# Kernel optimization log

Hardware: AMD Instinct MI355X
Metric: run time of the kernel (lower is better)

## Reference

```python
import jax, jax.numpy as jnp
import numpy as np

B, T, P = 256, 1024, 32
HOME = 0  # home_idx from init_kwargs


def setup_inputs() -> dict:
    key = jax.random.key(0)
    k1, k2 = jax.random.split(key, 2)
    U = jax.random.normal(k1, (B, T, P), dtype=jnp.float32)
    A = jax.random.uniform(k2, (P, P), dtype=jnp.float32, minval=-0.01, maxval=0.01)
    bias = jnp.zeros((P,), dtype=jnp.float32)
    return {"unary_logits_btp": U, "A": A, "bias": bias}


def reference(unary_logits_btp, A, bias):
    """Constrained Viterbi decode (enforce at least one non-home state).
    State is (purpose p, visited-nonhome flag v in {0,1}). Returns paths (B,T) int32."""
    U = unary_logits_btp + bias  # (B,T,P), bias broadcast as in decode()
    Bn, Tn, Pn = U.shape
    NEG = jnp.finfo(U.dtype).min / 4
    is_home = jnp.arange(Pn) == HOME  # (P,)

    # t=0: v=0 only at home, v=1 only at non-home
    d0 = jnp.where(is_home, U[:, 0], NEG)
    d1 = jnp.where(is_home, NEG, U[:, 0])
    delta0 = jnp.stack([d0, d1], axis=-1)  # (B,P,2)

    def step(delta, U_t):
        # prev{v}[b, q, p] = delta[b, q, v] + A[q, p]
        prev0 = delta[:, :, 0][:, :, None] + A  # (B,P,P)
        prev1 = delta[:, :, 1][:, :, None] + A
        a0 = jnp.argmax(prev0, axis=1).astype(jnp.int32)
        v0 = jnp.max(prev0, axis=1)  # (B,P)
        a1 = jnp.argmax(prev1, axis=1).astype(jnp.int32)
        v1 = jnp.max(prev1, axis=1)
        use1 = v1 > v0  # strict >, matching torch.where(val_from1 > val_from0, ...)
        bval = jnp.where(use1, v1, v0)
        bq = jnp.where(use1, a1, a0)
        bv = use1.astype(jnp.int32)
        # next v=0 reachable only at home (from prev v=0)
        dn0 = jnp.where(is_home, v0 + U_t, NEG)
        # next v=1: home from prev v=1; non-home from best of prev v=0/v=1
        dn1 = jnp.where(is_home, v1, bval) + U_t
        p1 = jnp.where(is_home, a1, bq)
        vv1 = jnp.where(is_home, 1, bv).astype(jnp.int32)
        delta_new = jnp.stack([dn0, dn1], axis=-1)          # (B,P,2)
        psi_p = jnp.stack([a0, p1], axis=-1)                # (B,P,2) best prev purpose
        psi_v = jnp.stack([jnp.zeros_like(vv1), vv1], -1)   # (B,P,2) best prev flag
        return delta_new, (psi_p, psi_v)

    Us = jnp.swapaxes(U, 0, 1)  # (T,B,P)
    delta_T, (psi_p, psi_v) = jax.lax.scan(step, delta0, Us[1:])  # psi_*: (T-1,B,P,2)

    last_p = jnp.argmax(delta_T[:, :, 1], axis=1).astype(jnp.int32)  # (B,)
    b_idx = jnp.arange(Bn)

    def back(carry, psi):
        y, v = carry  # (B,), (B,)
        pp, pv = psi  # (B,P,2)
        py = pp[b_idx, y, v]
        nv = pv[b_idx, y, v]
        return (py, nv), py

    _, ys = jax.lax.scan(back, (last_p, jnp.ones((Bn,), jnp.int32)), (psi_p, psi_v),
                         reverse=True)  # ys: (T-1,B) with ys[t] = y[t]
    paths = jnp.concatenate([jnp.swapaxes(ys, 0, 1), last_p[:, None]], axis=1)  # (B,T)
    return paths
```

## Files before the change

### kernel.cpp

```cpp
#include <hip/hip_runtime.h>

#define T_LEN 1024
#define P_DIM 32
#define HOME_IDX 0
#define NCHUNK 32
#define CHUNK 32


__launch_bounds__(1024, 1)
__global__ void crf_viterbi_kernel(const float* __restrict__ U,
                                   const float* __restrict__ A,
                                   const float* __restrict__ bias,
                                   int* __restrict__ out)
{
    __shared__ unsigned char spsi[(T_LEN - 1) * P_DIM];
    __shared__ unsigned char Mmap[NCHUNK * P_DIM];
    __shared__ unsigned char ent[NCHUNK];
    __shared__ int last_p_sh;

    const int tid = threadIdx.x;
    const int b   = blockIdx.x;
    int* __restrict__ outb = out + (size_t)b * T_LEN;

    if (tid < 64) {
        const int lane = tid;
        const int p    = lane & 31;
        const int h    = lane >> 5;
        const float NEG = -(3.4028234663852886e38f / 4.0f);

        float Areg[16];
#pragma unroll
        for (int j = 0; j < 16; ++j)
            Areg[j] = A[(16 * h + j) * P_DIM + p];
        const float A0p    = A[p];
        const float A00    = A[0];
        const float bias_p = bias[p];
        const float bias0  = bias[0];
        const int   qb     = h << 6;
        const bool  is_home = (p == HOME_IDX);

        const float* __restrict__ Ub = U + (size_t)b * T_LEN * P_DIM;

        const float u00 = Ub[p] + bias_p;
        float delta1  = is_home ? NEG : u00;
        float delta0h = Ub[HOME_IDX] + bias0;

        float L0 = Ub[1 * P_DIM + p];
        float L1 = Ub[2 * P_DIM + p];
        float L2 = Ub[3 * P_DIM + p];
        float L3 = Ub[4 * P_DIM + p];

        float Ut_n = L0 + bias_p;
        float u0_n = __shfl(Ut_n, 0);

#define STEP(t, Lc, Lr) do {                                                   \
    const float Ut  = Ut_n;                                                    \
    const float u0c = u0_n;                                                    \
    Ut_n = (Lc) + bias_p;                                                      \
    u0_n = __shfl(Ut_n, 0);                                                    \
    { int tn = (t) + 4; if (tn > T_LEN - 1) tn = T_LEN - 1;                    \
      (Lr) = Ub[(size_t)tn * P_DIM + p]; }                                     \
    const int dsrc = __float_as_int(delta1);                                   \
    float c[16];                                                               \
    _Pragma("unroll")                                                          \
    for (int j = 0; j < 16; ++j)                                               \
        c[j] = __int_as_float(__builtin_amdgcn_ds_bpermute(qb + 4 * j, dsrc))  \
               + Areg[j];                                                      \
                           \
    const float g0 = fmaxf(fmaxf(c[0],  c[1]),  c[2]);                         \
    const float g1 = fmaxf(fmaxf(c[3],  c[4]),  c[5]);                         \
    const float g2 = fmaxf(fmaxf(c[6],  c[7]),  c[8]);                         \
    const float g3 = fmaxf(fmaxf(c[9],  c[10]), c[11]);                        \
    const float g4 = fmaxf(fmaxf(c[12], c[13]), c[14]);                        \
    const float h0 = fmaxf(fmaxf(g0, g1), g2);                                 \
    const float h1 = fmaxf(fmaxf(g3, g4), c[15]);                              \
    const float bv = fmaxf(h0, h1);                                            \
    const float ovv = __shfl_xor(bv, 32);                                      \
    const float v1  = fmaxf(bv, ovv);                                          \
    const float v0  = delta0h + A0p;                                           \
    const bool  use1 = (v1 > v0);                    \
    const bool  cond = use1 || is_home;                                        \
    const float sel  = cond ? v1 : v0;                                         \
    const float dn1  = sel + Ut;                                               \
    delta0h = (delta0h + A00) + u0c;                                           \
                 \
    int ia = 99;                                                               \
    _Pragma("unroll")                                                          \
    for (int j = 15; j >= 0; --j)                                              \
        if (c[j] == v1) ia = (qb >> 2) + j;                                    \
    const int oia = __shfl_xor(ia, 32);                                        \
    const int a1  = (ia < oia) ? ia : oia;                                     \
    const int bt  = cond ? (a1 | 32) : 0;                                      \
    spsi[(size_t)((t) - 1) * P_DIM + p] = (unsigned char)bt;                   \
    delta1 = dn1;                                                              \
} while (0)

        STEP(1, L1, L0);
        STEP(2, L2, L1);
        STEP(3, L3, L2);
        for (int t = 4; t <= T_LEN - 4; t += 4) {
            STEP(t + 0, L0, L3);
            STEP(t + 1, L1, L0);
            STEP(t + 2, L2, L1);
            STEP(t + 3, L3, L2);
        }
#undef STEP

        float mv = delta1;
        int   mi = p;
#pragma unroll
        for (int m = 16; m >= 1; m >>= 1) {
            float ov = __shfl_xor(mv, m);
            int   oi = __shfl_xor(mi, m);
            bool take = (ov > mv) || ((ov == mv) && (oi < mi));
            mv = take ? ov : mv;
            mi = take ? oi : mi;
        }
        if (lane == 0) {
            outb[T_LEN - 1] = mi;
            last_p_sh = mi;
        }
    }

    __syncthreads();

    {
        const int c  = tid >> 5;
        const int pp = tid & 31;
        const int i_hi = min((c + 1) * CHUNK, T_LEN - 1);
        const int i_lo = c * CHUNK;
        int y = pp, v = 1;
        for (int i = i_hi - 1; i >= i_lo; --i) {
            const int bt = spsi[i * P_DIM + y];
            const int py = v ? (bt & 31) : 0;
            const int nv = v ? ((bt >> 5) & 1) : 0;
            y = py; v = nv;
        }
        Mmap[c * P_DIM + pp] = (unsigned char)(y | (v << 5));
    }
    __syncthreads();

    if (tid == 0) {
        int y = last_p_sh, v = 1;
        for (int c = NCHUNK - 1; c >= 0; --c) {
            ent[c] = (unsigned char)(y | (v << 5));
            if (v) {
                const int m = Mmap[c * P_DIM + y];
                y = m & 31;
                v = (m >> 5) & 1;
            } else {
                y = 0; v = 0;
            }
        }
    }
    __syncthreads();

    if (tid < NCHUNK) {
        const int c = tid;
        const int i_hi = min((c + 1) * CHUNK, T_LEN - 1);
        const int i_lo = c * CHUNK;
        const int e = ent[c];
        int y = e & 31;
        int v = (e >> 5) & 1;
        for (int i = i_hi - 1; i >= i_lo; --i) {
            const int bt = spsi[i * P_DIM + y];
            const int py = v ? (bt & 31) : 0;
            const int nv = v ? ((bt >> 5) & 1) : 0;
            outb[i] = py;
            y = py; v = nv;
        }
    }
}

extern "C" void kernel_launch(void* const* d_in, const int* in_sizes, int n_in,
                              void* d_out, int out_size, void* d_ws, size_t ws_size,
                              hipStream_t stream) {
    const float* U    = (const float*)d_in[0];
    const float* A    = (const float*)d_in[1];
    const float* bias = (const float*)d_in[2];
    int* out = (int*)d_out;

    const int B = in_sizes[0] / (T_LEN * P_DIM);
    crf_viterbi_kernel<<<B, 1024, 0, stream>>>(U, A, bias, out);
}
```

Measured before the change: 338.5 us.

## Broadcast delta via shared-memory float4 reads instead of bpermute split across half-waves

Each lane now holds the full 32-entry column of A and reads the whole previous delta vector from LDS as eight float4 loads, replacing the 16 ds_bpermute operations and the cross-half-wave max/argmax shuffles. It also issues the next step's LDS reads right after computing dn1, so they can overlap with the argmax scan. The cost is twice the max/compare work per lane and more registers. Lanes 32-63 still run and write the same LDS values redundantly, and the same-wave write-then-read ordering relies on LDS accesses completing in order without a barrier.

```diff
diff --git a/kernel.cpp b/kernel.cpp
--- a/kernel.cpp
+++ b/kernel.cpp
@@ -13,6 +13,7 @@
                                    const float* __restrict__ bias,
                                    int* __restrict__ out)
 {
+    __shared__ __align__(16) float4 sdelta[P_DIM / 4];
     __shared__ unsigned char spsi[(T_LEN - 1) * P_DIM];
     __shared__ unsigned char Mmap[NCHUNK * P_DIM];
     __shared__ unsigned char ent[NCHUNK];
@@ -25,18 +26,16 @@
     if (tid < 64) {
         const int lane = tid;
         const int p    = lane & 31;
-        const int h    = lane >> 5;
         const float NEG = -(3.4028234663852886e38f / 4.0f);
 
-        float Areg[16];
+        float Areg[32];
 #pragma unroll
-        for (int j = 0; j < 16; ++j)
-            Areg[j] = A[(16 * h + j) * P_DIM + p];
-        const float A0p    = A[p];
+        for (int q = 0; q < 32; ++q)
+            Areg[q] = A[q * P_DIM + p];
+        const float A0p    = Areg[0];
         const float A00    = A[0];
         const float bias_p = bias[p];
         const float bias0  = bias[0];
-        const int   qb     = h << 6;
         const bool  is_home = (p == HOME_IDX);
 
         const float* __restrict__ Ub = U + (size_t)b * T_LEN * P_DIM;
@@ -53,6 +52,10 @@
         float Ut_n = L0 + bias_p;
         float u0_n = __shfl(Ut_n, 0);
 
+        ((float*)sdelta)[p] = delta1;
+        float4 R0 = sdelta[0], R1 = sdelta[1], R2 = sdelta[2], R3 = sdelta[3];
+        float4 R4 = sdelta[4], R5 = sdelta[5], R6 = sdelta[6], R7 = sdelta[7];
+
 #define STEP(t, Lc, Lr) do {                                                   \
     const float Ut  = Ut_n;                                                    \
     const float u0c = u0_n;                                                    \
@@ -60,38 +63,47 @@
     u0_n = __shfl(Ut_n, 0);                                                    \
     { int tn = (t) + 4; if (tn > T_LEN - 1) tn = T_LEN - 1;                    \
       (Lr) = Ub[(size_t)tn * P_DIM + p]; }                                     \
-    const int dsrc = __float_as_int(delta1);                                   \
-    float c[16];                                                               \
-    _Pragma("unroll")                                                          \
-    for (int j = 0; j < 16; ++j)                                               \
-        c[j] = __int_as_float(__builtin_amdgcn_ds_bpermute(qb + 4 * j, dsrc))  \
-               + Areg[j];                                                      \
-                           \
+    float c[32];                                                               \
+    c[0]=R0.x+Areg[0];  c[1]=R0.y+Areg[1];  c[2]=R0.z+Areg[2];  c[3]=R0.w+Areg[3];   \
+    c[4]=R1.x+Areg[4];  c[5]=R1.y+Areg[5];  c[6]=R1.z+Areg[6];  c[7]=R1.w+Areg[7];   \
+    c[8]=R2.x+Areg[8];  c[9]=R2.y+Areg[9];  c[10]=R2.z+Areg[10]; c[11]=R2.w+Areg[11];\
+    c[12]=R3.x+Areg[12]; c[13]=R3.y+Areg[13]; c[14]=R3.z+Areg[14]; c[15]=R3.w+Areg[15];\
+    c[16]=R4.x+Areg[16]; c[17]=R4.y+Areg[17]; c[18]=R4.z+Areg[18]; c[19]=R4.w+Areg[19];\
+    c[20]=R5.x+Areg[20]; c[21]=R5.y+Areg[21]; c[22]=R5.z+Areg[22]; c[23]=R5.w+Areg[23];\
+    c[24]=R6.x+Areg[24]; c[25]=R6.y+Areg[25]; c[26]=R6.z+Areg[26]; c[27]=R6.w+Areg[27];\
+    c[28]=R7.x+Areg[28]; c[29]=R7.y+Areg[29]; c[30]=R7.z+Areg[30]; c[31]=R7.w+Areg[31];\
+                 \
     const float g0 = fmaxf(fmaxf(c[0],  c[1]),  c[2]);                         \
     const float g1 = fmaxf(fmaxf(c[3],  c[4]),  c[5]);                         \
     const float g2 = fmaxf(fmaxf(c[6],  c[7]),  c[8]);                         \
     const float g3 = fmaxf(fmaxf(c[9],  c[10]), c[11]);                        \
     const float g4 = fmaxf(fmaxf(c[12], c[13]), c[14]);                        \
-    const float h0 = fmaxf(fmaxf(g0, g1), g2);                                 \
-    const float h1 = fmaxf(fmaxf(g3, g4), c[15]);                              \
-    const float bv = fmaxf(h0, h1);                                            \
-    const float ovv = __shfl_xor(bv, 32);                                      \
-    const float v1  = fmaxf(bv, ovv);                                          \
-    const float v0  = delta0h + A0p;                                           \
+    const float g5 = fmaxf(fmaxf(c[15], c[16]), c[17]);                        \
+    const float g6 = fmaxf(fmaxf(c[18], c[19]), c[20]);                        \
+    const float g7 = fmaxf(fmaxf(c[21], c[22]), c[23]);                        \
+    const float g8 = fmaxf(fmaxf(c[24], c[25]), c[26]);                        \
+    const float g9 = fmaxf(fmaxf(c[27], c[28]), c[29]);                        \
+    const float s0 = fmaxf(fmaxf(g0, g1), g2);                                 \
+    const float s1 = fmaxf(fmaxf(g3, g4), g5);                                 \
+    const float s2 = fmaxf(fmaxf(g6, g7), g8);                                 \
+    const float s3 = fmaxf(fmaxf(g9, c[30]), c[31]);                           \
+    const float v1 = fmaxf(fmaxf(s0, s1), fmaxf(s2, s3));                      \
+    const float v0 = delta0h + A0p;                                            \
     const bool  use1 = (v1 > v0);                    \
     const bool  cond = use1 || is_home;                                        \
     const float sel  = cond ? v1 : v0;                                         \
     const float dn1  = sel + Ut;                                               \
     delta0h = (delta0h + A00) + u0c;                                           \
-                 \
-    int ia = 99;                                                               \
+      \
+    ((float*)sdelta)[p] = dn1;                                                 \
+    R0 = sdelta[0]; R1 = sdelta[1]; R2 = sdelta[2]; R3 = sdelta[3];            \
+    R4 = sdelta[4]; R5 = sdelta[5]; R6 = sdelta[6]; R7 = sdelta[7];            \
+      \
+    int ia = 0;                                                                \
     _Pragma("unroll")                                                          \
-    for (int j = 15; j >= 0; --j)                                              \
-        if (c[j] == v1) ia = (qb >> 2) + j;                                    \
-    const int oia = __shfl_xor(ia, 32);                                        \
-    const int a1  = (ia < oia) ? ia : oia;                                     \
-    const int bt  = cond ? (a1 | 32) : 0;                                      \
-    spsi[(size_t)((t) - 1) * P_DIM + p] = (unsigned char)bt;                   \
+    for (int j = 31; j >= 0; --j)                                              \
+        if (c[j] == v1) ia = j;                                                \
+    spsi[(size_t)((t) - 1) * P_DIM + p] = (unsigned char)(cond ? (ia | 32) : 0); \
     delta1 = dn1;                                                              \
 } while (0)
 
```

New measurement: 373.5 us. +10.3%, slower.
